# Kernel tuning notes

Hardware: AMD Instinct MI355X
Metric: run time of the kernel (lower is better)

## Reference

```python
import jax, jax.numpy as jnp
import numpy as np

B, N, DIM, H, DH = 2, 2048, 1024, 16, 64
SOFTCAP = 50.0
SCALE = DH ** -0.5
EPS = 1e-12


def _rmsnorm(x, gamma):
    # F.normalize (l2norm over last dim) * sqrt(dim) * (gamma + 1)
    norm = jnp.maximum(jnp.linalg.norm(x, axis=-1, keepdims=True), EPS)
    return (x / norm) * (DIM ** 0.5) * (gamma + 1.0)


def _rotate_half(t):
    # interleaved pairs: (x1, x2) -> (-x2, x1), as in rotary_embedding_torch
    t = t.reshape(*t.shape[:-1], -1, 2)
    x1, x2 = t[..., 0], t[..., 1]
    return jnp.stack((-x2, x1), axis=-1).reshape(*t.shape[:-2], -1)


def _apply_rotary(freqs, t):
    # freqs: [n, d] broadcast over [b, h, n, d]
    return t * jnp.cos(freqs) + _rotate_half(t) * jnp.sin(freqs)


def setup_inputs() -> dict:
    key = jax.random.key(0)
    k0, k1, k2, k3, k4 = jax.random.split(key, 5)
    x = jax.random.normal(k0, (B, N, DIM), jnp.float32)
    gamma = jax.random.normal(k1, (DIM,), jnp.float32) * 0.02
    w_qkv = jax.random.normal(k2, (DIM, 3 * H * DH), jnp.float32) * 0.02
    w_out = jax.random.normal(k3, (H * DH, DIM), jnp.float32) * 0.02
    rotary_emb = jax.random.normal(k4, (N, DH), jnp.float32)
    attn_mask = jnp.broadcast_to(jnp.tril(jnp.ones((N, N), bool)), (B, N, N))
    return {"x": x, "attn_mask": attn_mask, "rotary_emb": rotary_emb,
            "gamma": gamma, "w_qkv": w_qkv, "w_out": w_out}


def reference(x, attn_mask, rotary_emb, gamma, w_qkv, w_out):
    x = _rmsnorm(x, gamma)
    qkv = (x @ w_qkv).reshape(B, N, 3, H, DH)        # b n (qkv h d)
    qkv = jnp.transpose(qkv, (2, 0, 3, 1, 4))        # qkv b h n d
    q, k, v = qkv[0], qkv[1], qkv[2]
    q = _apply_rotary(rotary_emb, q)
    k = _apply_rotary(rotary_emb, k)
    q = q * SCALE
    sim = jnp.einsum('bhid,bhjd->bhij', q, k)
    sim = jnp.tanh(sim / SOFTCAP) * SOFTCAP          # softclamp
    mask_value = -jnp.finfo(sim.dtype).max
    sim = jnp.where(attn_mask[:, None, :, :], sim, mask_value)
    attn = jax.nn.softmax(sim, axis=-1)
    out = jnp.einsum('bhij,bhjd->bhid', attn, v)
    out = jnp.transpose(out, (0, 2, 1, 3)).reshape(B, N, H * DH)  # b n (h d)
    return out @ w_out
```

## Files before the change

### kernel.cpp

```cpp
#include <hip/hip_runtime.h>
#include <hip/hip_bf16.h>

typedef unsigned short u16;
typedef unsigned int u32;
typedef __bf16 bf16x8 __attribute__((ext_vector_type(8)));
typedef float f32x4 __attribute__((ext_vector_type(4)));

#define NB 2
#define NSEQ 2048
#define NDIM 1024
#define NH 16
#define NDH 64

static __device__ __forceinline__ u16 f2bf(float f) {
  return __builtin_bit_cast(u16, (__bf16)f);
}
static __device__ __forceinline__ float bf2f(u16 u) {
  union { u32 u; float f; } a; a.u = ((u32)u) << 16; return a.f;
}
static __device__ __forceinline__ bf16x8 ldbf8(const u16* p) {
  return *(const bf16x8*)p;
}
static __device__ __forceinline__ f32x4 mfma16(bf16x8 a, bf16x8 b, f32x4 c) {
  return __builtin_amdgcn_mfma_f32_16x16x32_bf16(a, b, c, 0, 0, 0);
}
static __device__ __forceinline__ float fexp2(float x) {
  return __builtin_amdgcn_exp2f(x);
}
#define GLDS(g, d) __builtin_amdgcn_global_load_lds(                         \
    (const __attribute__((address_space(1))) void*)(g),                      \
    (__attribute__((address_space(3))) void*)(d), 16, 0, 0)

__global__ __launch_bounds__(256) void k_transpose(const float* __restrict__ in,
                                                   u16* __restrict__ out,
                                                   int R, int C) {
  __shared__ u16 tile[64][65];
  const int r0 = blockIdx.x * 64, c0 = blockIdx.y * 64;
  const int t = threadIdx.x;
  const int tr = t >> 6;
  const int tc = t & 63;
#pragma unroll 4
  for (int p = 0; p < 16; p++) {
    int r = p * 4 + tr;
    tile[r][tc] = f2bf(in[(size_t)(r0 + r) * C + (c0 + tc)]);
  }
  __syncthreads();
#pragma unroll 4
  for (int p = 0; p < 16; p++) {
    int rr = p * 4 + tr;
    out[(size_t)(c0 + rr) * R + (r0 + tc)] = tile[tc][rr];
  }
}

__global__ __launch_bounds__(256) void k_rmsnorm(const float* __restrict__ x,
                                                 const float* __restrict__ gamma,
                                                 u16* __restrict__ xn) {
  __shared__ float part[4];
  const int row = blockIdx.x;
  const int t = threadIdx.x;
  const float4 v = ((const float4*)(x + (size_t)row * NDIM))[t];
  float ss = v.x * v.x + v.y * v.y + v.z * v.z + v.w * v.w;
#pragma unroll
  for (int off = 1; off < 64; off <<= 1) ss += __shfl_xor(ss, off, 64);
  if ((t & 63) == 0) part[t >> 6] = ss;
  __syncthreads();
  const float tot = part[0] + part[1] + part[2] + part[3];
  const float scale = 32.0f / fmaxf(sqrtf(tot), 1e-12f);
  const float4 g = ((const float4*)gamma)[t];
  u16 o0 = f2bf(v.x * scale * (g.x + 1.0f));
  u16 o1 = f2bf(v.y * scale * (g.y + 1.0f));
  u16 o2 = f2bf(v.z * scale * (g.z + 1.0f));
  u16 o3 = f2bf(v.w * scale * (g.w + 1.0f));
  uint2 pv;
  pv.x = (u32)o0 | ((u32)o1 << 16);
  pv.y = (u32)o2 | ((u32)o3 << 16);
  *(uint2*)(xn + (size_t)row * NDIM + t * 4) = pv;
}

template <int EPI, int BM, int BN>
__global__ __launch_bounds__(256) void k_gemm_bt(const u16* __restrict__ A,
                                                 const u16* __restrict__ BT,
                                                 float* __restrict__ Of,
                                                 u16* __restrict__ O0,
                                                 u16* __restrict__ O1,
                                                 u16* __restrict__ O2) {
  constexpr int KD = 1024, BK = 64, NT = KD / BK;
  constexpr int MI = BM / 32, NI = BN / 32;
  constexpr int AI = BM / 32, BI = BN / 32;
  __shared__ u16 As[BM * BK];
  __shared__ u16 Bs[BN * BK];
  const int m0 = blockIdx.x * BM, n0 = blockIdx.y * BN;
  const int t = threadIdx.x;
  const int w = t >> 6, l = t & 63, lo = l & 15, hi = l >> 4;
  const int wr = (w >> 1) * (BM / 2), wc = (w & 1) * (BN / 2);
  const int rl = l >> 3;
  const int sc8 = ((l & 7) ^ rl) * 8;
  const u16* agp[AI];
  u16* asd[AI];
#pragma unroll
  for (int i = 0; i < AI; i++) {
    const int ii = w * AI + i;
    agp[i] = A + (size_t)(m0 + ii * 8 + rl) * KD + sc8;
    asd[i] = (u16*)As + ii * 512;
  }
  const u16* bgp[BI];
  u16* bsd[BI];
#pragma unroll
  for (int i = 0; i < BI; i++) {
    const int ii = w * BI + i;
    bgp[i] = BT + (size_t)(n0 + ii * 8 + rl) * KD + sc8;
    bsd[i] = (u16*)Bs + ii * 512;
  }
  f32x4 acc[MI][NI] = {};

  for (int kt = 0; kt < NT; kt++) {
    const int k0 = kt * BK;
    __syncthreads();
#pragma unroll
    for (int i = 0; i < AI; i++) GLDS(agp[i] + k0, asd[i]);
#pragma unroll
    for (int i = 0; i < BI; i++) GLDS(bgp[i] + k0, bsd[i]);
    __syncthreads();
    bf16x8 af[MI][2], bb[NI][2];
#pragma unroll
    for (int i = 0; i < MI; i++) {
      const int Ra = wr + i * 16 + lo, xa = Ra & 7;
      af[i][0] = ldbf8(&As[Ra * 64 + ((hi ^ xa) << 3)]);
      af[i][1] = ldbf8(&As[Ra * 64 + (((4 + hi) ^ xa) << 3)]);
    }
#pragma unroll
    for (int j = 0; j < NI; j++) {
      const int Rb = wc + j * 16 + lo, xb = Rb & 7;
      bb[j][0] = ldbf8(&Bs[Rb * 64 + ((hi ^ xb) << 3)]);
      bb[j][1] = ldbf8(&Bs[Rb * 64 + (((4 + hi) ^ xb) << 3)]);
    }
#pragma unroll
    for (int i = 0; i < MI; i++)
#pragma unroll
      for (int j = 0; j < NI; j++) {
        acc[i][j] = mfma16(af[i][0], bb[j][0], acc[i][j]);
        acc[i][j] = mfma16(af[i][1], bb[j][1], acc[i][j]);
      }
  }

#pragma unroll
  for (int i = 0; i < MI; i++) {
#pragma unroll
    for (int j = 0; j < NI; j++) {
      const int gr0 = m0 + wr + i * 16 + hi * 4;
      const int gc = n0 + wc + j * 16 + lo;
#pragma unroll
      for (int r = 0; r < 4; r++) {
        const int row = gr0 + r;
        if (EPI == 0) {
          Of[(size_t)row * 1024 + gc] = acc[i][j][r];
        } else {
          const u16 bv = f2bf(acc[i][j][r]);
          const int which = gc >> 10, rem = gc & 1023;
          const int h = rem >> 6, dh = rem & 63;
          const int b = row >> 11, ns = row & 2047;
          if (which == 2) {
            O2[(((size_t)b * NH + h) * NDH + dh) * NSEQ + ns] = bv;
          } else {
            const size_t idx = ((((size_t)b * NH + h) * NSEQ) + ns) * NDH + dh;
            (which == 0 ? O0 : O1)[idx] = bv;
          }
        }
      }
    }
  }
}

__global__ __launch_bounds__(256) void k_rotary(u16* __restrict__ qb,
                                                u16* __restrict__ kb,
                                                const float* __restrict__ rot) {
  const int gi = blockIdx.x * 256 + threadIdx.x;
  const int half = gi >> 19;
  const int i = gi & ((1 << 19) - 1);
  u16* buf = half ? kb : qb;
  const float scale = half ? 1.0f : 0.125f;
  const int d0 = (i & 7) * 8;
  const int n = (i >> 3) & (NSEQ - 1);
  union { uint4 v; u16 s[8]; } u;
  u.v = *(const uint4*)(buf + (size_t)i * 8);
  float fr[8];
  *(float4*)&fr[0] = *(const float4*)(rot + n * NDH + d0);
  *(float4*)&fr[4] = *(const float4*)(rot + n * NDH + d0 + 4);
  union { uint4 v; u16 s[8]; } o;
#pragma unroll
  for (int p = 0; p < 4; p++) {
    float a = bf2f(u.s[2 * p]), b = bf2f(u.s[2 * p + 1]);
    float s0, c0, s1, c1;
    __sincosf(fr[2 * p], &s0, &c0);
    __sincosf(fr[2 * p + 1], &s1, &c1);
    o.s[2 * p] = f2bf((a * c0 - b * s0) * scale);
    o.s[2 * p + 1] = f2bf((b * c1 + a * s1) * scale);
  }
  *(uint4*)(buf + (size_t)i * 8) = o.v;
}

#define KCH(row, ch) ((((ch) ^ ((row) & 7)) * 8))
__global__ __launch_bounds__(256, 4) void k_attn(const u16* __restrict__ Q,
                                                 const u16* __restrict__ K,
                                                 const u16* __restrict__ Vt,
                                                 u16* __restrict__ O) {
  __shared__ u16 Ks[2][4096];
  __shared__ u16 Vs[2][4096];
  __shared__ u16 Ps[4][16][64];
  const int pr = blockIdx.x >> 5;
  const int bh = blockIdx.x & 31;
  const int b = bh >> 4, h = bh & 15;
  const size_t base = (size_t)bh * (NSEQ * NDH);
  const int t = threadIdx.x;
  const int w = t >> 6, l = t & 63, lo = l & 15, hi = l >> 4;

  const int rl = l >> 3;
  const int sc8 = ((l & 7) ^ rl) * 8;
  const size_t vtb = (size_t)bh * NDH * NSEQ;

#define STAGE(bb, kt_)                                                        \
  {                                                                           \
    _Pragma("unroll")                                                         \
    for (int i_ = 0; i_ < 2; i_++) {                                          \
      const int ii = w * 2 + i_;                                              \
      const int R_ = ii * 8 + rl;                                             \
      GLDS(K + base + (size_t)((kt_) * 64 + R_) * NDH + sc8,                  \
           &Ks[bb][ii * 512]);                                                \
      GLDS(Vt + vtb + (size_t)R_ * NSEQ + (kt_) * 64 + sc8,                   \
           &Vs[bb][ii * 512]);                                                \
    }                                                                         \
  }

  int cur = 0;
  STAGE(0, 0);

#pragma unroll
  for (int half = 0; half < 2; half++) {
    const int qt = half ? (31 - pr) : pr;
    const int q0 = qt * 64;
    bf16x8 aq0, aq1;
    {
      const u16* qp = Q + base + (size_t)(q0 + w * 16 + lo) * NDH;
      aq0 = ldbf8(qp + hi * 8);
      aq1 = ldbf8(qp + 32 + hi * 8);
    }
    f32x4 accO[4] = {};
    float l_part[4] = {0.f, 0.f, 0.f, 0.f};
    const int nkt = qt + 1;
    const int ktd = qt;
    const int rowg = q0 + w * 16 + hi * 4;

    for (int kt = 0; kt < nkt; kt++) {
      __syncthreads();
      if (kt + 1 < nkt) {
        STAGE(cur ^ 1, kt + 1);
      } else if (half == 0) {
        STAGE(cur ^ 1, 0);
      }

      const u16* ks = Ks[cur];
      const u16* vs = Vs[cur];
      f32x4 s[4];
#pragma unroll
      for (int nt = 0; nt < 4; nt++) {
        const int kr = nt * 16 + lo;
        f32x4 z = {};
        z = mfma16(aq0, ldbf8(&ks[kr * 64 + KCH(kr, hi)]), z);
        z = mfma16(aq1, ldbf8(&ks[kr * 64 + KCH(kr, 4 + hi)]), z);
        s[nt] = z;
      }
      const bool diag = (kt == ktd);
#pragma unroll
      for (int nt = 0; nt < 4; nt++) {
        const int col = kt * 64 + nt * 16 + lo;
#pragma unroll
        for (int r = 0; r < 4; r++) {
          const float v = s[nt][r];
          const float u = v * v;
          float p = fexp2(v * fmaf(u, fmaf(u, 3.0777855e-8f,
                                           -1.9235932e-4f), 1.44269504f));
          if (diag && col > rowg + r) p = 0.0f;
          s[nt][r] = p;
          l_part[r] += p;
        }
      }
#pragma unroll
      for (int nt = 0; nt < 4; nt++)
#pragma unroll
        for (int r = 0; r < 4; r++) {
          const int row = hi * 4 + r;
          Ps[w][row][KCH(row, 2 * nt + (lo >> 3)) + (lo & 7)] = f2bf(s[nt][r]);
        }

      const bf16x8 ap0 = ldbf8(&Ps[w][lo][KCH(lo, hi)]);
      const bf16x8 ap1 = ldbf8(&Ps[w][lo][KCH(lo, 4 + hi)]);
#pragma unroll
      for (int dt = 0; dt < 4; dt++) {
        const int d = dt * 16 + lo;
        accO[dt] = mfma16(ap0, ldbf8(&vs[d * 64 + KCH(d, hi)]), accO[dt]);
        accO[dt] = mfma16(ap1, ldbf8(&vs[d * 64 + KCH(d, 4 + hi)]), accO[dt]);
      }
      cur ^= 1;
    }
    float lr[4];
#pragma unroll
    for (int r = 0; r < 4; r++) {
      float lv = l_part[r];
      lv += __shfl_xor(lv, 1, 64);
      lv += __shfl_xor(lv, 2, 64);
      lv += __shfl_xor(lv, 4, 64);
      lv += __shfl_xor(lv, 8, 64);
      lr[r] = __builtin_amdgcn_rcpf(lv);
    }
#pragma unroll
    for (int dt = 0; dt < 4; dt++) {
#pragma unroll
      for (int r = 0; r < 4; r++) {
        const int row = rowg + r;
        const float v = accO[dt][r] * lr[r];
        const size_t idx = (((size_t)(b * NSEQ + row)) * NH + h) * NDH + dt * 16 + lo;
        O[idx] = f2bf(v);
      }
    }
  }
#undef STAGE
}

extern "C" void kernel_launch(void* const* d_in, const int* in_sizes, int n_in,
                              void* d_out, int out_size, void* d_ws, size_t ws_size,
                              hipStream_t stream) {
  const float* x     = (const float*)d_in[0];
  const float* rot   = (const float*)d_in[2];
  const float* gamma = (const float*)d_in[3];
  const float* wqkv  = (const float*)d_in[4];
  const float* wout  = (const float*)d_in[5];

  char* ws = (char*)d_ws;
  u16* xn    = (u16*)(ws);
  u16* wqkvT = (u16*)(ws + (size_t)( 8u << 20));
  u16* woutT = (u16*)(ws + (size_t)(14u << 20));
  u16* qb    = (u16*)(ws + (size_t)(16u << 20));
  u16* kb    = (u16*)(ws + (size_t)(24u << 20));
  u16* vt    = (u16*)(ws + (size_t)(32u << 20));
  u16* ob    = xn;

  k_transpose<<<dim3(16, 48), 256, 0, stream>>>(wqkv, wqkvT, 1024, 3072);
  k_transpose<<<dim3(16, 16), 256, 0, stream>>>(wout, woutT, 1024, 1024);
  k_rmsnorm<<<4096, 256, 0, stream>>>(x, gamma, xn);
  k_gemm_bt<1, 64, 128><<<dim3(64, 24), 256, 0, stream>>>(xn, wqkvT, nullptr, qb, kb, vt);
  k_rotary<<<4096, 256, 0, stream>>>(qb, kb, rot);
  k_attn<<<512, 256, 0, stream>>>(qb, kb, vt, ob);
  k_gemm_bt<0, 64, 64><<<dim3(64, 16), 256, 0, stream>>>(ob, woutT, (float*)d_out, nullptr, nullptr, nullptr);
}
```

Before: 123.0 us.

## Fuse rotary embedding into QKV GEMM epilogue with precomputed cos/sin table

Removes the standalone rotary kernel and applies rotary and the query scaling inside the QKV GEMM epilogue. The partner element comes from a lane shuffle, and cos/sin are read from a table built by a small prep kernel. This saves a full read-modify-write pass over Q and K plus one launch. The QKV GEMM tile drops from 64x128 to 64x64 so that each block's columns fall inside a single one of Q, K or V. The rotary table shares workspace with woutT, so the wout transpose is moved after the QKV GEMM.

```diff
diff --git a/kernel.cpp b/kernel.cpp
--- a/kernel.cpp
+++ b/kernel.cpp
@@ -77,9 +77,18 @@
   *(uint2*)(xn + (size_t)row * NDIM + t * 4) = pv;
 }
 
+__global__ __launch_bounds__(256) void k_rotprep(const float* __restrict__ rot,
+                                                 float2* __restrict__ tab) {
+  const int i = blockIdx.x * 256 + threadIdx.x;
+  float s, c;
+  __sincosf(rot[i], &s, &c);
+  tab[i] = make_float2(c, s);
+}
+
 template <int EPI, int BM, int BN>
 __global__ __launch_bounds__(256) void k_gemm_bt(const u16* __restrict__ A,
                                                  const u16* __restrict__ BT,
+                                                 const float2* __restrict__ rtab,
                                                  float* __restrict__ Of,
                                                  u16* __restrict__ O0,
                                                  u16* __restrict__ O1,
@@ -143,6 +152,7 @@
       }
   }
 
+  const int which = (EPI == 1) ? (n0 >> 10) : 0;
 #pragma unroll
   for (int i = 0; i < MI; i++) {
 #pragma unroll
@@ -155,48 +165,23 @@
         if (EPI == 0) {
           Of[(size_t)row * 1024 + gc] = acc[i][j][r];
         } else {
-          const u16 bv = f2bf(acc[i][j][r]);
-          const int which = gc >> 10, rem = gc & 1023;
-          const int h = rem >> 6, dh = rem & 63;
+          const int h = (gc >> 6) & 15, dh = gc & 63;
           const int b = row >> 11, ns = row & 2047;
-          if (which == 2) {
-            O2[(((size_t)b * NH + h) * NDH + dh) * NSEQ + ns] = bv;
+          float v = acc[i][j][r];
+          if (which < 2) {
+            const float2 cs = rtab[(ns << 6) + dh];
+            const float pv = __shfl_xor(v, 1, 64);
+            float rv = fmaf((lo & 1) ? pv : -pv, cs.y, v * cs.x);
+            if (which == 0) rv *= 0.125f;
+            const size_t idx = ((((size_t)b * NH + h) * NSEQ) + ns) * NDH + dh;
+            (which == 0 ? O0 : O1)[idx] = f2bf(rv);
           } else {
-            const size_t idx = ((((size_t)b * NH + h) * NSEQ) + ns) * NDH + dh;
-            (which == 0 ? O0 : O1)[idx] = bv;
+            O2[(((size_t)b * NH + h) * NDH + dh) * NSEQ + ns] = f2bf(v);
           }
         }
       }
     }
   }
-}
-
-__global__ __launch_bounds__(256) void k_rotary(u16* __restrict__ qb,
-                                                u16* __restrict__ kb,
-                                                const float* __restrict__ rot) {
-  const int gi = blockIdx.x * 256 + threadIdx.x;
-  const int half = gi >> 19;
-  const int i = gi & ((1 << 19) - 1);
-  u16* buf = half ? kb : qb;
-  const float scale = half ? 1.0f : 0.125f;
-  const int d0 = (i & 7) * 8;
-  const int n = (i >> 3) & (NSEQ - 1);
-  union { uint4 v; u16 s[8]; } u;
-  u.v = *(const uint4*)(buf + (size_t)i * 8);
-  float fr[8];
-  *(float4*)&fr[0] = *(const float4*)(rot + n * NDH + d0);
-  *(float4*)&fr[4] = *(const float4*)(rot + n * NDH + d0 + 4);
-  union { uint4 v; u16 s[8]; } o;
-#pragma unroll
-  for (int p = 0; p < 4; p++) {
-    float a = bf2f(u.s[2 * p]), b = bf2f(u.s[2 * p + 1]);
-    float s0, c0, s1, c1;
-    __sincosf(fr[2 * p], &s0, &c0);
-    __sincosf(fr[2 * p + 1], &s1, &c1);
-    o.s[2 * p] = f2bf((a * c0 - b * s0) * scale);
-    o.s[2 * p + 1] = f2bf((b * c1 + a * s1) * scale);
-  }
-  *(uint4*)(buf + (size_t)i * 8) = o.v;
 }
 
 #define KCH(row, ch) ((((ch) ^ ((row) & 7)) * 8))
@@ -338,6 +323,7 @@
   char* ws = (char*)d_ws;
   u16* xn    = (u16*)(ws);
   u16* wqkvT = (u16*)(ws + (size_t)( 8u << 20));
+  float2* rtab = (float2*)(ws + (size_t)(14u << 20));
   u16* woutT = (u16*)(ws + (size_t)(14u << 20));
   u16* qb    = (u16*)(ws + (size_t)(16u << 20));
   u16* kb    = (u16*)(ws + (size_t)(24u << 20));
@@ -345,10 +331,12 @@
   u16* ob    = xn;
 
   k_transpose<<<dim3(16, 48), 256, 0, stream>>>(wqkv, wqkvT, 1024, 3072);
+  k_rmsnorm<<<4096, 256, 0, stream>>>(x, gamma, xn);
+  k_rotprep<<<512, 256, 0, stream>>>(rot, rtab);
+  k_gemm_bt<1, 64, 64><<<dim3(64, 48), 256, 0, stream>>>(
+      xn, wqkvT, rtab, nullptr, qb, kb, vt);
   k_transpose<<<dim3(16, 16), 256, 0, stream>>>(wout, woutT, 1024, 1024);
-  k_rmsnorm<<<4096, 256, 0, stream>>>(x, gamma, xn);
-  k_gemm_bt<1, 64, 128><<<dim3(64, 24), 256, 0, stream>>>(xn, wqkvT, nullptr, qb, kb, vt);
-  k_rotary<<<4096, 256, 0, stream>>>(qb, kb, rot);
   k_attn<<<512, 256, 0, stream>>>(qb, kb, vt, ob);
-  k_gemm_bt<0, 64, 64><<<dim3(64, 16), 256, 0, stream>>>(ob, woutT, (float*)d_out, nullptr, nullptr, nullptr);
-}
+  k_gemm_bt<0, 64, 64><<<dim3(64, 16), 256, 0, stream>>>(
+      ob, woutT, nullptr, (float*)d_out, nullptr, nullptr, nullptr);
+}
```

Measured after the change: 130.1 us. 5.8% more time.
